# Optimization experiments

Hardware: AMD Instinct MI355X
Metric: run time of the kernel (lower is better)

## Reference

```python
import jax, jax.numpy as jnp
import numpy as np

N, NFEAT, NHID, NCLASS, E = 100000, 128, 128, 40, 1600000

def _glorot(key, fan_in, fan_out):
    lim = float(np.sqrt(6.0 / (fan_in + fan_out)))
    return jax.random.uniform(key, (fan_in, fan_out), jnp.float32, -lim, lim)

def setup_inputs() -> dict:
    key = jax.random.key(0)
    ks = jax.random.split(key, 20)
    inp = {
        'x': jax.random.normal(ks[0], (N, NFEAT), jnp.float32),
        'edge_index': jax.random.randint(ks[1], (2, E), 0, N, jnp.int64 if jax.config.x64_enabled else jnp.int32),
    }
    dims = [(NFEAT, NHID), (NHID, NHID), (NHID, NHID), (NHID, NHID), (NHID, NHID), (NHID, NHID)]
    names = ['gc1_w1', 'gc1_w2', 'gc2_w1', 'gc2_w2', 'gc3_w1', 'gc3_w2']
    for i, (nm, (fi, fo)) in enumerate(zip(names, dims)):
        inp[nm] = _glorot(ks[2 + i], fi, fo)
        inp[nm.replace('w', 'b')] = jnp.zeros((fo,), jnp.float32)
    inp['lin1_w'] = _glorot(ks[10], 3 * NHID, 3 * NHID)
    inp['lin1_b'] = jnp.zeros((3 * NHID,), jnp.float32)
    inp['lin2_w'] = _glorot(ks[11], 3 * NHID, NCLASS)
    inp['lin2_b'] = jnp.zeros((NCLASS,), jnp.float32)
    return inp

def _gin_conv(x, src, dst, w1, b1, w2, b2):
    # GINConv, eps=0: mlp(x + sum_{j->i} x_j)
    agg = jax.ops.segment_sum(x[src], dst, num_segments=N)  # [N, d]
    h = jax.nn.relu((x + agg) @ w1 + b1)
    return jax.nn.relu(h @ w2 + b2)

def reference(x, edge_index, gc1_w1, gc1_b1, gc1_w2, gc1_b2,
              gc2_w1, gc2_b1, gc2_w2, gc2_b2,
              gc3_w1, gc3_b1, gc3_w2, gc3_b2,
              lin1_w, lin1_b, lin2_w, lin2_b):
    src, dst = edge_index[0], edge_index[1]
    h1 = _gin_conv(x, src, dst, gc1_w1, gc1_b1, gc1_w2, gc1_b2)
    h2 = _gin_conv(h1, src, dst, gc2_w1, gc2_b1, gc2_w2, gc2_b2)
    h3 = _gin_conv(h2, src, dst, gc3_w1, gc3_b1, gc3_w2, gc3_b2)
    h = jnp.concatenate([h1, h2, h3], axis=1)  # [N, 3*nhid]
    h = jax.nn.relu(h @ lin1_w + lin1_b)  # dropout inactive in eval mode
    h = h @ lin2_w + lin2_b
    return jax.nn.log_softmax(h, axis=1)
```

## Files before the change

kernel.cpp:

```cpp
#include <hip/hip_runtime.h>

#define N_NODES 100000
#define NEDGE   1600000
#define NHID    128
#define NCLASS  40

#define AGG_NODES 128
#define COLV_LDS  3072
#define FILL_SLICES 8
#define FILL_RANGE  12500
#define WPREP_TOT   264192

using bf16x8 = __attribute__((ext_vector_type(8))) short;
using f32x4  = __attribute__((ext_vector_type(4))) float;

__device__ __forceinline__ float bf2f(unsigned short s) {
    unsigned u = ((unsigned)s) << 16; float f; __builtin_memcpy(&f, &u, 4); return f;
}
__device__ __forceinline__ unsigned short f2bf(float f) {
    unsigned u; __builtin_memcpy(&u, &f, 4);
    u = u + 0x7fffu + ((u >> 16) & 1u);
    return (unsigned short)(u >> 16);
}

__device__ __forceinline__ void gld16(const void* g, void* l) {
    __builtin_amdgcn_global_load_lds(g, l, 16, 0, 0);
}

__global__ void k_zero(int* __restrict__ p, int n) {
    int i = blockIdx.x * 256 + threadIdx.x;
    if (i < n) p[i] = 0;
}

__global__ __launch_bounds__(256) void k_countr(const int* __restrict__ ei, int* __restrict__ cnt) {
    int slice = blockIdx.x & 7;
    int e = (blockIdx.x >> 3) * 256 + threadIdx.x;
    if (e >= NEDGE) return;
    int d = ei[NEDGE + e];
    int lo = slice * FILL_RANGE;
    if (d >= lo && d < lo + FILL_RANGE) atomicAdd(&cnt[d], 1);
}

__global__ void k_scan1(const int* __restrict__ cnt, int* __restrict__ rp, int* __restrict__ bsum) {
    __shared__ int sh[256];
    int t = threadIdx.x, base = blockIdx.x * 1024;
    int v[4]; int s = 0;
    for (int k = 0; k < 4; ++k) { int i = base + t * 4 + k; v[k] = (i < N_NODES) ? cnt[i] : 0; s += v[k]; }
    sh[t] = s; __syncthreads();
    for (int off = 1; off < 256; off <<= 1) {
        int x = (t >= off) ? sh[t - off] : 0;
        __syncthreads();
        sh[t] += x;
        __syncthreads();
    }
    int excl = sh[t] - s;
    for (int k = 0; k < 4; ++k) { int i = base + t * 4 + k; if (i < N_NODES) rp[i] = excl; excl += v[k]; }
    if (t == 255) bsum[blockIdx.x] = sh[255];
}

__global__ void k_scan2(int* __restrict__ bsum, int nb) {
    __shared__ int sh[256];
    int t = threadIdx.x;
    int v = (t < nb) ? bsum[t] : 0;
    sh[t] = v; __syncthreads();
    for (int off = 1; off < 256; off <<= 1) {
        int x = (t >= off) ? sh[t - off] : 0;
        __syncthreads();
        sh[t] += x;
        __syncthreads();
    }
    if (t < nb) bsum[t] = sh[t] - v;
}

__global__ void k_scan3(int* __restrict__ rp, const int* __restrict__ bsum) {
    int base = blockIdx.x * 1024;
    int off = bsum[blockIdx.x];
    for (int k = 0; k < 4; ++k) {
        int i = base + threadIdx.x * 4 + k;
        if (i < N_NODES) rp[i] += off;
    }
    if (blockIdx.x == 0 && threadIdx.x == 0) rp[N_NODES] = NEDGE;
}

__global__ __launch_bounds__(256) void k_fillr(const int* __restrict__ ei, const int* __restrict__ rp,
                                               int* __restrict__ cur, int* __restrict__ colv) {
    int slice = blockIdx.x & 7;
    int e = (blockIdx.x >> 3) * 256 + threadIdx.x;
    if (e >= NEDGE) return;
    int d = ei[NEDGE + e];
    int lo = slice * FILL_RANGE;
    if (d >= lo && d < lo + FILL_RANGE) {
        int p = atomicAdd(&cur[d], 1);
        colv[rp[d] + p] = ei[e];
    }
}

__global__ void k_wprep_all(const float* __restrict__ g0, const float* __restrict__ g1,
                            const float* __restrict__ g2, const float* __restrict__ g3,
                            const float* __restrict__ g4, const float* __restrict__ g5,
                            const float* __restrict__ l1w, const float* __restrict__ l2w,
                            unsigned short* __restrict__ dst) {
    int idx = blockIdx.x * 256 + threadIdx.x;
    if (idx >= WPREP_TOT) return;
    const float* w; int local, K, O;
    if (idx < 98304) {
        int r = idx >> 14; local = idx & 16383; K = 128; O = 128;
        w = r == 0 ? g0 : r == 1 ? g1 : r == 2 ? g2 : r == 3 ? g3 : r == 4 ? g4 : g5;
    } else if (idx < 245760) {
        local = idx - 98304; K = 384; O = 384; w = l1w;
    } else {
        local = idx - 245760; K = 384; O = 40; w = l2w;
    }
    int kss = K >> 5;
    int e = local & 7, lane = (local >> 3) & 63, rest = local >> 9;
    int ks = rest % kss, ot = rest / kss;
    int c = ot * 16 + (lane & 15);
    int k = ks * 32 + (lane >> 4) * 8 + e;
    float v = (c < O) ? w[k * O + c] : 0.f;
    dst[idx] = f2bf(v);
}

__global__ void k_xprep(const float* __restrict__ x, unsigned short* __restrict__ xs) {
    int s = blockIdx.x & 7;
    int rest = (blockIdx.x >> 3) * 256 + threadIdx.x;
    if (rest >= N_NODES * 8) return;
    int n = rest >> 3, wrd = rest & 7;
    float2 v = *(const float2*)(x + (size_t)n * 128 + s * 16 + wrd * 2);
    ((unsigned*)xs)[(size_t)s * N_NODES * 8 + rest] =
        (unsigned)f2bf(v.x) | ((unsigned)f2bf(v.y) << 16);
}

__device__ __forceinline__ void acc8(float* acc, uint4 f, float m) {
    unsigned u[4] = {f.x, f.y, f.z, f.w};
    for (int d = 0; d < 4; ++d) {
        acc[2 * d]     = fmaf(m, bf2f((unsigned short)u[d]), acc[2 * d]);
        acc[2 * d + 1] = fmaf(m, bf2f((unsigned short)(u[d] >> 16)), acc[2 * d + 1]);
    }
}

__global__ __launch_bounds__(256) void k_aggs(const unsigned short* __restrict__ feat,
                                              unsigned short* __restrict__ tout,
                                              const int* __restrict__ rp,
                                              const int* __restrict__ colv) {
    __shared__ int scol[COLV_LDS];
    __shared__ int srp[AGG_NODES + 1];
    const int s = blockIdx.x & 7;
    const int chunk = blockIdx.x >> 3;
    const int tid = threadIdx.x;
    const int nbase = chunk * AGG_NODES;

    for (int i = tid; i <= AGG_NODES; i += 256) {
        int n = nbase + i;
        srp[i] = rp[n <= N_NODES ? n : N_NODES];
    }
    __syncthreads();
    const int ebase = srp[0];
    const int ecount = srp[AGG_NODES] - ebase;
    const int elds = ecount < COLV_LDS ? ecount : COLV_LDS;
    for (int i = tid; i < elds; i += 256) scol[i] = colv[ebase + i];
    __syncthreads();

    const unsigned* fs = (const unsigned*)feat + (size_t)s * N_NODES * 8;
    unsigned* ts = (unsigned*)tout + (size_t)s * N_NODES * 8;

    const int sub = tid >> 1, half = tid & 1;
    const int node = nbase + sub;
    if (node >= N_NODES) return;
    const int off = half * 4;
    const int e0 = srp[sub] - ebase, e1 = srp[sub + 1] - ebase;

    float acc[8];
    {
        uint4 a = *(const uint4*)(fs + (size_t)node * 8 + off);
        unsigned u[4] = {a.x, a.y, a.z, a.w};
        for (int d = 0; d < 4; ++d) {
            acc[2 * d]     = bf2f((unsigned short)u[d]);
            acc[2 * d + 1] = bf2f((unsigned short)(u[d] >> 16));
        }
    }

    for (int e = e0; e < e1; e += 8) {
        int j[8]; float m[8];
        #pragma unroll
        for (int k = 0; k < 8; ++k) {
            int ee = e + k;
            bool v = ee < e1;
            int idx = ee < COLV_LDS ? scol[ee] : colv[ebase + ee];
            j[k] = v ? idx : node;
            m[k] = v ? 1.f : 0.f;
        }
        uint4 f[8];
        #pragma unroll
        for (int k = 0; k < 8; ++k)
            f[k] = *(const uint4*)(fs + (size_t)j[k] * 8 + off);
        #pragma unroll
        for (int k = 0; k < 8; ++k) acc8(acc, f[k], m[k]);
    }

    uint4 o;
    o.x = (unsigned)f2bf(acc[0]) | ((unsigned)f2bf(acc[1]) << 16);
    o.y = (unsigned)f2bf(acc[2]) | ((unsigned)f2bf(acc[3]) << 16);
    o.z = (unsigned)f2bf(acc[4]) | ((unsigned)f2bf(acc[5]) << 16);
    o.w = (unsigned)f2bf(acc[6]) | ((unsigned)f2bf(acc[7]) << 16);
    *(uint4*)(ts + (size_t)node * 8 + off) = o;
}

__global__ __launch_bounds__(256) void k_mlp(
    const unsigned short* __restrict__ tin,
    const unsigned short* __restrict__ w1t, const float* __restrict__ b1,
    const unsigned short* __restrict__ w2t, const float* __restrict__ b2,
    unsigned short* __restrict__ hout) {
    __shared__ __align__(16) char tlds[64 * 256];
    __shared__ __align__(16) char hlds[64 * 256];
    const int tid = threadIdx.x, lane = tid & 63, w = tid >> 6;
    const int l15 = lane & 15, lg = lane >> 4;
    const int nbase = blockIdx.x * 64;

    #pragma unroll
    for (int i = 0; i < 4; ++i) {
        int byte = w * 4096 + i * 1024 + lane * 16;
        int r = byte >> 8, c8s = (byte >> 4) & 15;
        int c8 = c8s ^ (r & 7);
        int slice = c8 >> 1, half = c8 & 1;
        int node = nbase + r; if (node >= N_NODES) node = 0;
        gld16(tin + ((size_t)slice * N_NODES + node) * 16 + half * 8,
              tlds + w * 4096 + i * 1024);
    }

    bf16x8 B1[2][4]; float bias1[2]; int cols[2];
    #pragma unroll
    for (int ot = 0; ot < 2; ++ot) {
        int c = (w * 2 + ot) * 16 + l15;
        cols[ot] = c; bias1[ot] = b1[c];
        #pragma unroll
        for (int ks = 0; ks < 4; ++ks)
            B1[ot][ks] = *(const bf16x8*)(w1t + ((size_t)((w * 2 + ot) * 4 + ks) * 64 + lane) * 8);
    }
    bf16x8 B2[2][4]; float bias2[2];
    #pragma unroll
    for (int ot = 0; ot < 2; ++ot) {
        bias2[ot] = b2[(w * 2 + ot) * 16 + l15];
        #pragma unroll
        for (int ks = 0; ks < 4; ++ks)
            B2[ot][ks] = *(const bf16x8*)(w2t + ((size_t)((w * 2 + ot) * 4 + ks) * 64 + lane) * 8);
    }
    __syncthreads();

    {
        bf16x8 A[2][4];
        #pragma unroll
        for (int ks = 0; ks < 4; ++ks)
            A[0][ks] = *(const bf16x8*)(tlds + l15 * 256 + ((ks * 64 + lg * 16) ^ ((l15 & 7) << 4)));
        #pragma unroll
        for (int m = 0; m < 4; ++m) {
            int cur = m & 1, nxt = cur ^ 1;
            if (m < 3) {
                int row = (m + 1) * 16 + l15;
                #pragma unroll
                for (int ks = 0; ks < 4; ++ks)
                    A[nxt][ks] = *(const bf16x8*)(tlds + row * 256 + ((ks * 64 + lg * 16) ^ ((row & 7) << 4)));
            }
            #pragma unroll
            for (int ot = 0; ot < 2; ++ot) {
                f32x4 acc = {0.f, 0.f, 0.f, 0.f};
                #pragma unroll
                for (int ks = 0; ks < 4; ++ks)
                    acc = __builtin_amdgcn_mfma_f32_16x16x32_bf16(A[cur][ks], B1[ot][ks], acc, 0, 0, 0);
                int c2 = cols[ot] * 2;
                #pragma unroll
                for (int r = 0; r < 4; ++r) {
                    int row = m * 16 + lg * 4 + r;
                    float v = acc[r] + bias1[ot]; v = v > 0.f ? v : 0.f;
                    *(unsigned short*)(hlds + row * 256 + (c2 ^ ((row & 7) << 4))) = f2bf(v);
                }
            }
        }
    }
    __syncthreads();

    {
        bf16x8 A[2][4];
        #pragma unroll
        for (int ks = 0; ks < 4; ++ks)
            A[0][ks] = *(const bf16x8*)(hlds + l15 * 256 + ((ks * 64 + lg * 16) ^ ((l15 & 7) << 4)));
        #pragma unroll
        for (int m = 0; m < 4; ++m) {
            int cur = m & 1, nxt = cur ^ 1;
            if (m < 3) {
                int row = (m + 1) * 16 + l15;
                #pragma unroll
                for (int ks = 0; ks < 4; ++ks)
                    A[nxt][ks] = *(const bf16x8*)(hlds + row * 256 + ((ks * 64 + lg * 16) ^ ((row & 7) << 4)));
            }
            #pragma unroll
            for (int ot = 0; ot < 2; ++ot) {
                f32x4 acc = {0.f, 0.f, 0.f, 0.f};
                #pragma unroll
                for (int ks = 0; ks < 4; ++ks)
                    acc = __builtin_amdgcn_mfma_f32_16x16x32_bf16(A[cur][ks], B2[ot][ks], acc, 0, 0, 0);
                int cslice = cols[ot] >> 4, cw = cols[ot] & 15;
                #pragma unroll
                for (int r = 0; r < 4; ++r) {
                    int node = nbase + m * 16 + lg * 4 + r;
                    if (node < N_NODES) {
                        float v = acc[r] + bias2[ot]; v = v > 0.f ? v : 0.f;
                        hout[((size_t)cslice * N_NODES + node) * 16 + cw] = f2bf(v);
                    }
                }
            }
        }
    }
}

__global__ __launch_bounds__(512, 2) void k_final(
    const unsigned short* __restrict__ h1, const unsigned short* __restrict__ h2,
    const unsigned short* __restrict__ h3,
    const unsigned short* __restrict__ l1t, const float* __restrict__ l1b,
    const unsigned short* __restrict__ l2t, const float* __restrict__ l2b,
    float* __restrict__ out) {
    extern __shared__ __align__(16) char lds[];
    const int tid = threadIdx.x, lane = tid & 63, w = tid >> 6;
    const int l15 = lane & 15, lg = lane >> 4;
    const int nbase = blockIdx.x * 128;

    #pragma unroll
    for (int i = 0; i < 12; ++i) {
        unsigned byte = (unsigned)(w * 12288 + i * 1024 + lane * 16);
        unsigned r = byte / 768u;
        unsigned rem = byte - r * 768u;
        int c8 = (int)(rem >> 4) ^ (int)(r & 7);
        int part = c8 >> 4, c8p = c8 & 15;
        int slice = c8p >> 1, half = c8p & 1;
        int node = nbase + (int)r; if (node >= N_NODES) node = 0;
        const unsigned short* hp = part == 0 ? h1 : (part == 1 ? h2 : h3);
        gld16(hp + ((size_t)slice * N_NODES + node) * 16 + half * 8,
              lds + w * 12288 + i * 1024);
    }

    bf16x8 B[3][3];
    #pragma unroll
    for (int ot = 0; ot < 3; ++ot) {
        B[0][ot] = *(const bf16x8*)(l1t + ((size_t)((w * 3 + ot) * 12 + 0) * 64 + lane) * 8);
        B[1][ot] = *(const bf16x8*)(l1t + ((size_t)((w * 3 + ot) * 12 + 1) * 64 + lane) * 8);
    }
    __syncthreads();

    f32x4 acc[8][3];
    #pragma unroll
    for (int m = 0; m < 8; ++m)
        #pragma unroll
        for (int ot = 0; ot < 3; ++ot) acc[m][ot] = {0.f, 0.f, 0.f, 0.f};
    {
        #pragma unroll
        for (int ks = 0; ks < 12; ++ks) {
            int cur = ks % 3;
            if (ks < 10) {
                int nx2 = (ks + 2) % 3;
                #pragma unroll
                for (int ot = 0; ot < 3; ++ot)
                    B[nx2][ot] = *(const bf16x8*)(l1t + ((size_t)((w * 3 + ot) * 12 + ks + 2) * 64 + lane) * 8);
            }
            bf16x8 A[8];
            #pragma unroll
            for (int m = 0; m < 8; ++m) {
                int row = m * 16 + l15;
                A[m] = *(const bf16x8*)(lds + row * 768 + ((ks * 64 + lg * 16) ^ ((row & 7) << 4)));
            }
            #pragma unroll
            for (int ot = 0; ot < 3; ++ot)
                #pragma unroll
                for (int m = 0; m < 8; ++m)
                    acc[m][ot] = __builtin_amdgcn_mfma_f32_16x16x32_bf16(A[m], B[cur][ot], acc[m][ot], 0, 0, 0);
        }
    }
    __syncthreads();

    #pragma unroll
    for (int ot = 0; ot < 3; ++ot) {
        int c = (w * 3 + ot) * 16 + l15;
        float bias = l1b[c];
        #pragma unroll
        for (int m = 0; m < 8; ++m)
            #pragma unroll
            for (int r = 0; r < 4; ++r) {
                int row = m * 16 + lg * 4 + r;
                float v = acc[m][ot][r] + bias; v = v > 0.f ? v : 0.f;
                *(unsigned short*)(lds + row * 768 + ((c * 2) ^ ((row & 7) << 4))) = f2bf(v);
            }
    }
    __syncthreads();

    f32x4 acc2[3];
    #pragma unroll
    for (int ot = 0; ot < 3; ++ot) acc2[ot] = {0.f, 0.f, 0.f, 0.f};
    {
        const int row = w * 16 + l15;
        bf16x8 C2[2][3]; bf16x8 A2[2];
        #pragma unroll
        for (int ot = 0; ot < 3; ++ot)
            C2[0][ot] = *(const bf16x8*)(l2t + ((size_t)(ot * 12) * 64 + lane) * 8);
        A2[0] = *(const bf16x8*)(lds + row * 768 + ((lg * 16) ^ ((row & 7) << 4)));
        #pragma unroll
        for (int ks = 0; ks < 12; ++ks) {
            int cur = ks & 1, nxt = cur ^ 1;
            if (ks < 11) {
                #pragma unroll
                for (int ot = 0; ot < 3; ++ot)
                    C2[nxt][ot] = *(const bf16x8*)(l2t + ((size_t)(ot * 12 + ks + 1) * 64 + lane) * 8);
                A2[nxt] = *(const bf16x8*)(lds + row * 768 + (((ks + 1) * 64 + lg * 16) ^ ((row & 7) << 4)));
            }
            #pragma unroll
            for (int ot = 0; ot < 3; ++ot)
                acc2[ot] = __builtin_amdgcn_mfma_f32_16x16x32_bf16(A2[cur], C2[cur][ot], acc2[ot], 0, 0, 0);
        }
    }

    int c0 = l15;
    #pragma unroll
    for (int r = 0; r < 4; ++r) {
        float v0 = acc2[0][r] + l2b[c0];
        float v1 = acc2[1][r] + l2b[c0 + 16];
        float v2 = (c0 < 8) ? (acc2[2][r] + l2b[c0 + 32]) : -1e30f;
        float mx = fmaxf(fmaxf(v0, v1), v2);
        for (int msk = 1; msk < 16; msk <<= 1) mx = fmaxf(mx, __shfl_xor(mx, msk));
        float s = __expf(v0 - mx) + __expf(v1 - mx) + ((c0 < 8) ? __expf(v2 - mx) : 0.f);
        for (int msk = 1; msk < 16; msk <<= 1) s += __shfl_xor(s, msk);
        float lse = mx + __logf(s);
        int node = nbase + w * 16 + lg * 4 + r;
        if (node < N_NODES) {
            out[(size_t)node * 40 + c0] = v0 - lse;
            out[(size_t)node * 40 + c0 + 16] = v1 - lse;
            if (c0 < 8) out[(size_t)node * 40 + c0 + 32] = v2 - lse;
        }
    }
}

extern "C" void kernel_launch(void* const* d_in, const int* in_sizes, int n_in,
                              void* d_out, int out_size, void* d_ws, size_t ws_size,
                              hipStream_t stream) {
    const float* x  = (const float*)d_in[0];
    const int*   ei = (const int*)d_in[1];
    const float* gw1[3] = {(const float*)d_in[2],  (const float*)d_in[6],  (const float*)d_in[10]};
    const float* gb1[3] = {(const float*)d_in[3],  (const float*)d_in[7],  (const float*)d_in[11]};
    const float* gw2[3] = {(const float*)d_in[4],  (const float*)d_in[8],  (const float*)d_in[12]};
    const float* gb2[3] = {(const float*)d_in[5],  (const float*)d_in[9],  (const float*)d_in[13]};
    const float* l1w = (const float*)d_in[14];
    const float* l1b = (const float*)d_in[15];
    const float* l2w = (const float*)d_in[16];
    const float* l2b = (const float*)d_in[17];
    float* out = (float*)d_out;

    char* p = (char*)d_ws;
    auto alloc = [&](size_t bytes) { char* q = p; p += (bytes + 255) & ~(size_t)255; return q; };
    int* rp   = (int*)alloc(4 * (N_NODES + 1));
    int* cnt  = (int*)alloc(4 * N_NODES);
    int* bsum = (int*)alloc(4 * 256);
    int* colv = (int*)alloc(4 * (size_t)NEDGE);
    unsigned short* t  = (unsigned short*)alloc(2 * (size_t)N_NODES * 128);
    unsigned short* h1 = (unsigned short*)alloc(2 * (size_t)N_NODES * 128);
    unsigned short* h2 = (unsigned short*)alloc(2 * (size_t)N_NODES * 128);
    unsigned short* h3 = (unsigned short*)alloc(2 * (size_t)N_NODES * 128);
    unsigned short* xs = h3;
    unsigned short* wt[6];
    for (int i = 0; i < 6; ++i) wt[i] = (unsigned short*)alloc(2 * 128 * 128);
    unsigned short* l1t = (unsigned short*)alloc(2 * 384 * 384);
    unsigned short* l2t = (unsigned short*)alloc(2 * 48 * 384);

    static bool attr_set = false;
    if (!attr_set) {
        hipFuncSetAttribute((const void*)k_final,
                            hipFuncAttributeMaxDynamicSharedMemorySize, 128 * 768);
        attr_set = true;
    }

    const int nb = (N_NODES + 1023) / 1024;
    k_zero<<<(N_NODES + 255) / 256, 256, 0, stream>>>(cnt, N_NODES);
    k_countr<<<((NEDGE + 255) / 256) * FILL_SLICES, 256, 0, stream>>>(ei, cnt);
    k_scan1<<<nb, 256, 0, stream>>>(cnt, rp, bsum);
    k_scan2<<<1, 256, 0, stream>>>(bsum, nb);
    k_scan3<<<nb, 256, 0, stream>>>(rp, bsum);
    k_zero<<<(N_NODES + 255) / 256, 256, 0, stream>>>(cnt, N_NODES);
    k_fillr<<<((NEDGE + 255) / 256) * FILL_SLICES, 256, 0, stream>>>(ei, rp, cnt, colv);

    k_wprep_all<<<(WPREP_TOT + 255) / 256, 256, 0, stream>>>(
        gw1[0], gw2[0], gw1[1], gw2[1], gw1[2], gw2[2], l1w, l2w, wt[0]);

    k_xprep<<<8 * ((N_NODES * 8 + 255) / 256), 256, 0, stream>>>(x, xs);

    const int gagg = ((N_NODES + AGG_NODES - 1) / AGG_NODES) * 8;
    const int gtile = (N_NODES + 63) / 64;
    const int gtile2 = (N_NODES + 127) / 128;
    k_aggs<<<gagg, 256, 0, stream>>>(xs, t, rp, colv);
    k_mlp<<<gtile, 256, 0, stream>>>(t, wt[0], gb1[0], wt[1], gb2[0], h1);
    k_aggs<<<gagg, 256, 0, stream>>>(h1, t, rp, colv);
    k_mlp<<<gtile, 256, 0, stream>>>(t, wt[2], gb1[1], wt[3], gb2[1], h2);
    k_aggs<<<gagg, 256, 0, stream>>>(h2, t, rp, colv);
    k_mlp<<<gtile, 256, 0, stream>>>(t, wt[4], gb1[2], wt[5], gb2[2], h3);
    k_final<<<gtile2, 512, 128 * 768, stream>>>(h1, h2, h3, l1t, l1b, l2t, l2b, out);
}
```

Before: 508.3 us.

## Retile MLP to 128 nodes/512 threads, fast-path aggregation, simplify CSR fill

The MLP kernel now processes 128 nodes per block with 8 waves, each wave owning one 16-column output slice instead of two. This halves per-wave weight registers and doubles the row tiles each wave iterates. The aggregation kernel gains a fast path when all edges fit in LDS, dropping the per-edge bounds check and global fallback for full groups of 8. CSR construction drops two zero kernels: scan3 writes cursor offsets directly, and fillr uses the atomic result as the absolute position, with a memset replacing the first zero kernel.

```diff
diff --git a/kernel.cpp b/kernel.cpp
--- a/kernel.cpp
+++ b/kernel.cpp
@@ -25,11 +25,6 @@
 
 __device__ __forceinline__ void gld16(const void* g, void* l) {
     __builtin_amdgcn_global_load_lds(g, l, 16, 0, 0);
-}
-
-__global__ void k_zero(int* __restrict__ p, int n) {
-    int i = blockIdx.x * 256 + threadIdx.x;
-    if (i < n) p[i] = 0;
 }
 
 __global__ __launch_bounds__(256) void k_countr(const int* __restrict__ ei, int* __restrict__ cnt) {
@@ -72,17 +67,17 @@
     if (t < nb) bsum[t] = sh[t] - v;
 }
 
-__global__ void k_scan3(int* __restrict__ rp, const int* __restrict__ bsum) {
+__global__ void k_scan3(int* __restrict__ rp, const int* __restrict__ bsum, int* __restrict__ cur) {
     int base = blockIdx.x * 1024;
     int off = bsum[blockIdx.x];
     for (int k = 0; k < 4; ++k) {
         int i = base + threadIdx.x * 4 + k;
-        if (i < N_NODES) rp[i] += off;
+        if (i < N_NODES) { int v = rp[i] + off; rp[i] = v; cur[i] = v; }
     }
     if (blockIdx.x == 0 && threadIdx.x == 0) rp[N_NODES] = NEDGE;
 }
 
-__global__ __launch_bounds__(256) void k_fillr(const int* __restrict__ ei, const int* __restrict__ rp,
+__global__ __launch_bounds__(256) void k_fillr(const int* __restrict__ ei,
                                                int* __restrict__ cur, int* __restrict__ colv) {
     int slice = blockIdx.x & 7;
     int e = (blockIdx.x >> 3) * 256 + threadIdx.x;
@@ -91,7 +86,7 @@
     int lo = slice * FILL_RANGE;
     if (d >= lo && d < lo + FILL_RANGE) {
         int p = atomicAdd(&cur[d], 1);
-        colv[rp[d] + p] = ei[e];
+        colv[p] = ei[e];
     }
 }
 
@@ -142,7 +137,7 @@
                                               unsigned short* __restrict__ tout,
                                               const int* __restrict__ rp,
                                               const int* __restrict__ colv) {
-    __shared__ int scol[COLV_LDS];
+    __shared__ int scol[COLV_LDS + 8];
     __shared__ int srp[AGG_NODES + 1];
     const int s = blockIdx.x & 7;
     const int chunk = blockIdx.x >> 3;
@@ -158,6 +153,7 @@
     const int ecount = srp[AGG_NODES] - ebase;
     const int elds = ecount < COLV_LDS ? ecount : COLV_LDS;
     for (int i = tid; i < elds; i += 256) scol[i] = colv[ebase + i];
+    if (tid < 8) scol[elds + tid] = 0;
     __syncthreads();
 
     const unsigned* fs = (const unsigned*)feat + (size_t)s * N_NODES * 8;
@@ -179,22 +175,54 @@
         }
     }
 
-    for (int e = e0; e < e1; e += 8) {
-        int j[8]; float m[8];
-        #pragma unroll
-        for (int k = 0; k < 8; ++k) {
-            int ee = e + k;
-            bool v = ee < e1;
-            int idx = ee < COLV_LDS ? scol[ee] : colv[ebase + ee];
-            j[k] = v ? idx : node;
-            m[k] = v ? 1.f : 0.f;
-        }
-        uint4 f[8];
-        #pragma unroll
-        for (int k = 0; k < 8; ++k)
-            f[k] = *(const uint4*)(fs + (size_t)j[k] * 8 + off);
-        #pragma unroll
-        for (int k = 0; k < 8; ++k) acc8(acc, f[k], m[k]);
+    if (ecount <= COLV_LDS) {
+        int e = e0;
+        const int efull = e0 + ((e1 - e0) & ~7);
+        for (; e < efull; e += 8) {
+            int j[8];
+            #pragma unroll
+            for (int k = 0; k < 8; ++k) j[k] = scol[e + k];
+            uint4 f[8];
+            #pragma unroll
+            for (int k = 0; k < 8; ++k)
+                f[k] = *(const uint4*)(fs + (size_t)j[k] * 8 + off);
+            #pragma unroll
+            for (int k = 0; k < 8; ++k) acc8(acc, f[k], 1.f);
+        }
+        if (e < e1) {
+            int j[8]; float m[8];
+            #pragma unroll
+            for (int k = 0; k < 8; ++k) {
+                int ee = e + k;
+                bool v = ee < e1;
+                j[k] = v ? scol[ee] : node;
+                m[k] = v ? 1.f : 0.f;
+            }
+            uint4 f[8];
+            #pragma unroll
+            for (int k = 0; k < 8; ++k)
+                f[k] = *(const uint4*)(fs + (size_t)j[k] * 8 + off);
+            #pragma unroll
+            for (int k = 0; k < 8; ++k) acc8(acc, f[k], m[k]);
+        }
+    } else {
+        for (int e = e0; e < e1; e += 8) {
+            int j[8]; float m[8];
+            #pragma unroll
+            for (int k = 0; k < 8; ++k) {
+                int ee = e + k;
+                bool v = ee < e1;
+                int idx = ee < COLV_LDS ? scol[ee] : colv[ebase + ee];
+                j[k] = v ? idx : node;
+                m[k] = v ? 1.f : 0.f;
+            }
+            uint4 f[8];
+            #pragma unroll
+            for (int k = 0; k < 8; ++k)
+                f[k] = *(const uint4*)(fs + (size_t)j[k] * 8 + off);
+            #pragma unroll
+            for (int k = 0; k < 8; ++k) acc8(acc, f[k], m[k]);
+        }
     }
 
     uint4 o;
@@ -205,44 +233,35 @@
     *(uint4*)(ts + (size_t)node * 8 + off) = o;
 }
 
-__global__ __launch_bounds__(256) void k_mlp(
+__global__ __launch_bounds__(512) void k_mlp(
     const unsigned short* __restrict__ tin,
     const unsigned short* __restrict__ w1t, const float* __restrict__ b1,
     const unsigned short* __restrict__ w2t, const float* __restrict__ b2,
     unsigned short* __restrict__ hout) {
-    __shared__ __align__(16) char tlds[64 * 256];
-    __shared__ __align__(16) char hlds[64 * 256];
+    __shared__ __align__(16) char tlds[128 * 256];
+    __shared__ __align__(16) char hlds[128 * 256];
     const int tid = threadIdx.x, lane = tid & 63, w = tid >> 6;
     const int l15 = lane & 15, lg = lane >> 4;
-    const int nbase = blockIdx.x * 64;
+    const int nbase = blockIdx.x * 128;
 
     #pragma unroll
     for (int i = 0; i < 4; ++i) {
-        int byte = w * 4096 + i * 1024 + lane * 16;
+        int byte = w * 1024 + i * 8192 + lane * 16;
         int r = byte >> 8, c8s = (byte >> 4) & 15;
         int c8 = c8s ^ (r & 7);
         int slice = c8 >> 1, half = c8 & 1;
         int node = nbase + r; if (node >= N_NODES) node = 0;
         gld16(tin + ((size_t)slice * N_NODES + node) * 16 + half * 8,
-              tlds + w * 4096 + i * 1024);
-    }
-
-    bf16x8 B1[2][4]; float bias1[2]; int cols[2];
-    #pragma unroll
-    for (int ot = 0; ot < 2; ++ot) {
-        int c = (w * 2 + ot) * 16 + l15;
-        cols[ot] = c; bias1[ot] = b1[c];
-        #pragma unroll
-        for (int ks = 0; ks < 4; ++ks)
-            B1[ot][ks] = *(const bf16x8*)(w1t + ((size_t)((w * 2 + ot) * 4 + ks) * 64 + lane) * 8);
-    }
-    bf16x8 B2[2][4]; float bias2[2];
-    #pragma unroll
-    for (int ot = 0; ot < 2; ++ot) {
-        bias2[ot] = b2[(w * 2 + ot) * 16 + l15];
-        #pragma unroll
-        for (int ks = 0; ks < 4; ++ks)
-            B2[ot][ks] = *(const bf16x8*)(w2t + ((size_t)((w * 2 + ot) * 4 + ks) * 64 + lane) * 8);
+              tlds + w * 1024 + i * 8192);
+    }
+
+    bf16x8 B1[4], B2[4];
+    const int col = w * 16 + l15;
+    const float bias1 = b1[col], bias2 = b2[col];
+    #pragma unroll
+    for (int ks = 0; ks < 4; ++ks) {
+        B1[ks] = *(const bf16x8*)(w1t + ((size_t)(w * 4 + ks) * 64 + lane) * 8);
+        B2[ks] = *(const bf16x8*)(w2t + ((size_t)(w * 4 + ks) * 64 + lane) * 8);
     }
     __syncthreads();
 
@@ -251,28 +270,25 @@
         #pragma unroll
         for (int ks = 0; ks < 4; ++ks)
             A[0][ks] = *(const bf16x8*)(tlds + l15 * 256 + ((ks * 64 + lg * 16) ^ ((l15 & 7) << 4)));
-        #pragma unroll
-        for (int m = 0; m < 4; ++m) {
+        const int c2 = col * 2;
+        #pragma unroll
+        for (int m = 0; m < 8; ++m) {
             int cur = m & 1, nxt = cur ^ 1;
-            if (m < 3) {
+            if (m < 7) {
                 int row = (m + 1) * 16 + l15;
                 #pragma unroll
                 for (int ks = 0; ks < 4; ++ks)
                     A[nxt][ks] = *(const bf16x8*)(tlds + row * 256 + ((ks * 64 + lg * 16) ^ ((row & 7) << 4)));
             }
-            #pragma unroll
-            for (int ot = 0; ot < 2; ++ot) {
-                f32x4 acc = {0.f, 0.f, 0.f, 0.f};
-                #pragma unroll
-                for (int ks = 0; ks < 4; ++ks)
-                    acc = __builtin_amdgcn_mfma_f32_16x16x32_bf16(A[cur][ks], B1[ot][ks], acc, 0, 0, 0);
-                int c2 = cols[ot] * 2;
-                #pragma unroll
-                for (int r = 0; r < 4; ++r) {
-                    int row = m * 16 + lg * 4 + r;
-                    float v = acc[r] + bias1[ot]; v = v > 0.f ? v : 0.f;
-                    *(unsigned short*)(hlds + row * 256 + (c2 ^ ((row & 7) << 4))) = f2bf(v);
-                }
+            f32x4 acc = {0.f, 0.f, 0.f, 0.f};
+            #pragma unroll
+            for (int ks = 0; ks < 4; ++ks)
+                acc = __builtin_amdgcn_mfma_f32_16x16x32_bf16(A[cur][ks], B1[ks], acc, 0, 0, 0);
+            #pragma unroll
+            for (int r = 0; r < 4; ++r) {
+                int row = m * 16 + lg * 4 + r;
+                float v = acc[r] + bias1; v = v > 0.f ? v : 0.f;
+                *(unsigned short*)(hlds + row * 256 + (c2 ^ ((row & 7) << 4))) = f2bf(v);
             }
         }
     }
@@ -284,28 +300,24 @@
         for (int ks = 0; ks < 4; ++ks)
             A[0][ks] = *(const bf16x8*)(hlds + l15 * 256 + ((ks * 64 + lg * 16) ^ ((l15 & 7) << 4)));
         #pragma unroll
-        for (int m = 0; m < 4; ++m) {
+        for (int m = 0; m < 8; ++m) {
             int cur = m & 1, nxt = cur ^ 1;
-            if (m < 3) {
+            if (m < 7) {
                 int row = (m + 1) * 16 + l15;
                 #pragma unroll
                 for (int ks = 0; ks < 4; ++ks)
                     A[nxt][ks] = *(const bf16x8*)(hlds + row * 256 + ((ks * 64 + lg * 16) ^ ((row & 7) << 4)));
             }
-            #pragma unroll
-            for (int ot = 0; ot < 2; ++ot) {
-                f32x4 acc = {0.f, 0.f, 0.f, 0.f};
-                #pragma unroll
-                for (int ks = 0; ks < 4; ++ks)
-                    acc = __builtin_amdgcn_mfma_f32_16x16x32_bf16(A[cur][ks], B2[ot][ks], acc, 0, 0, 0);
-                int cslice = cols[ot] >> 4, cw = cols[ot] & 15;
-                #pragma unroll
-                for (int r = 0; r < 4; ++r) {
-                    int node = nbase + m * 16 + lg * 4 + r;
-                    if (node < N_NODES) {
-                        float v = acc[r] + bias2[ot]; v = v > 0.f ? v : 0.f;
-                        hout[((size_t)cslice * N_NODES + node) * 16 + cw] = f2bf(v);
-                    }
+            f32x4 acc = {0.f, 0.f, 0.f, 0.f};
+            #pragma unroll
+            for (int ks = 0; ks < 4; ++ks)
+                acc = __builtin_amdgcn_mfma_f32_16x16x32_bf16(A[cur][ks], B2[ks], acc, 0, 0, 0);
+            #pragma unroll
+            for (int r = 0; r < 4; ++r) {
+                int node = nbase + m * 16 + lg * 4 + r;
+                if (node < N_NODES) {
+                    float v = acc[r] + bias2; v = v > 0.f ? v : 0.f;
+                    hout[((size_t)w * N_NODES + node) * 16 + l15] = f2bf(v);
                 }
             }
         }
@@ -454,6 +466,7 @@
     auto alloc = [&](size_t bytes) { char* q = p; p += (bytes + 255) & ~(size_t)255; return q; };
     int* rp   = (int*)alloc(4 * (N_NODES + 1));
     int* cnt  = (int*)alloc(4 * N_NODES);
+    int* cur  = (int*)alloc(4 * N_NODES);
     int* bsum = (int*)alloc(4 * 256);
     int* colv = (int*)alloc(4 * (size_t)NEDGE);
     unsigned short* t  = (unsigned short*)alloc(2 * (size_t)N_NODES * 128);
@@ -474,13 +487,12 @@
     }
 
     const int nb = (N_NODES + 1023) / 1024;
-    k_zero<<<(N_NODES + 255) / 256, 256, 0, stream>>>(cnt, N_NODES);
+    hipMemsetAsync(cnt, 0, 4 * N_NODES, stream);
     k_countr<<<((NEDGE + 255) / 256) * FILL_SLICES, 256, 0, stream>>>(ei, cnt);
     k_scan1<<<nb, 256, 0, stream>>>(cnt, rp, bsum);
     k_scan2<<<1, 256, 0, stream>>>(bsum, nb);
-    k_scan3<<<nb, 256, 0, stream>>>(rp, bsum);
-    k_zero<<<(N_NODES + 255) / 256, 256, 0, stream>>>(cnt, N_NODES);
-    k_fillr<<<((NEDGE + 255) / 256) * FILL_SLICES, 256, 0, stream>>>(ei, rp, cnt, colv);
+    k_scan3<<<nb, 256, 0, stream>>>(rp, bsum, cur);
+    k_fillr<<<((NEDGE + 255) / 256) * FILL_SLICES, 256, 0, stream>>>(ei, cur, colv);
 
     k_wprep_all<<<(WPREP_TOT + 255) / 256, 256, 0, stream>>>(
         gw1[0], gw2[0], gw1[1], gw2[1], gw1[2], gw2[2], l1w, l2w, wt[0]);
@@ -488,13 +500,12 @@
     k_xprep<<<8 * ((N_NODES * 8 + 255) / 256), 256, 0, stream>>>(x, xs);
 
     const int gagg = ((N_NODES + AGG_NODES - 1) / AGG_NODES) * 8;
-    const int gtile = (N_NODES + 63) / 64;
     const int gtile2 = (N_NODES + 127) / 128;
     k_aggs<<<gagg, 256, 0, stream>>>(xs, t, rp, colv);
-    k_mlp<<<gtile, 256, 0, stream>>>(t, wt[0], gb1[0], wt[1], gb2[0], h1);
+    k_mlp<<<gtile2, 512, 0, stream>>>(t, wt[0], gb1[0], wt[1], gb2[0], h1);
     k_aggs<<<gagg, 256, 0, stream>>>(h1, t, rp, colv);
-    k_mlp<<<gtile, 256, 0, stream>>>(t, wt[2], gb1[1], wt[3], gb2[1], h2);
+    k_mlp<<<gtile2, 512, 0, stream>>>(t, wt[2], gb1[1], wt[3], gb2[1], h2);
     k_aggs<<<gagg, 256, 0, stream>>>(h2, t, rp, colv);
-    k_mlp<<<gtile, 256, 0, stream>>>(t, wt[4], gb1[2], wt[5], gb2[2], h3);
+    k_mlp<<<gtile2, 512, 0, stream>>>(t, wt[4], gb1[2], wt[5], gb2[2], h3);
     k_final<<<gtile2, 512, 128 * 768, stream>>>(h1, h2, h3, l1t, l1b, l2t, l2b, out);
 }
```

Result: no change. 515.3 us (+1.4%).
